# Kernel optimization log

Hardware: AMD Instinct MI355X
Metric: run time of the kernel (lower is better)

## Reference

```python
import jax, jax.numpy as jnp
from jax import lax
import numpy as np

NBC, NAC, KF, RHO = 14, 45, 52, 0.05
KT = np.arange(0.8, 0, -1.0 / 64, dtype=np.float32)[None, :]  # (1, 52) AC kernel time axis
K = KT.shape[1]


def _sigm(x, off, slope):
    return jax.nn.sigmoid(slope * (x - off))


def _ac_kernel(log_tr, log_td, kt):
    tr = jnp.exp(log_tr)[:, None]  # (nAC,1)
    td = jnp.exp(log_td)[:, None]
    k = jnp.exp(-kt / td) - jnp.exp(-(td + tr) / (td * tr) * kt)  # (nAC,K)
    return k / jnp.linalg.norm(k, axis=1, keepdims=True)


def setup_inputs() -> dict:
    key = jax.random.key(0)
    ks = jax.random.split(key, 12)
    B, T = 64, 4096
    n = 0.01  # noise_init_scale
    return {
        "x": jax.random.normal(ks[0], (B, T), jnp.float32) * 0.5,
        "bc_kernels": jax.random.normal(ks[1], (NBC, KF), jnp.float32) * 0.1,
        "log_sigmoid_slope": jnp.log(2.0) + n * jax.random.normal(ks[2], (NBC,), jnp.float32),
        "sigmoid_offset": 1.5 + n * jax.random.normal(ks[3], (NBC,), jnp.float32),
        "log_bc_ac_weight": jnp.log(1.0 / NBC) + n * jax.random.normal(ks[4], (NAC, NBC), jnp.float32),
        "log_ac_tau_rise": jnp.log(0.1) + n * jax.random.normal(ks[5], (NAC,), jnp.float32),
        "log_ac_tau_decay": jnp.log(0.1) + n * jax.random.normal(ks[6], (NAC,), jnp.float32),
        "log_ac_sigmoid_slope": jnp.log(2.0) + n * jax.random.normal(ks[7], (NAC,), jnp.float32),
        "ac_sigmoid_offset": 1.5 + n * jax.random.normal(ks[8], (NAC,), jnp.float32),
        "log_ac_bc_weight": jnp.log(0.01) + n * jax.random.normal(ks[9], (NBC, NAC), jnp.float32),
        "out_scale": jnp.ones((NBC,), jnp.float32),
    }


def reference(x, bc_kernels, log_sigmoid_slope, sigmoid_offset, log_bc_ac_weight,
              log_ac_tau_rise, log_ac_tau_decay, log_ac_sigmoid_slope,
              ac_sigmoid_offset, log_ac_bc_weight, out_scale):
    B, T = x.shape
    kt = jnp.asarray(KT)
    # linear_filter: causal conv of stimulus with per-BC kernels -> (T, B, nBC)
    xf = lax.conv_general_dilated(x[:, None, :], bc_kernels[:, None, :], (1,), [(KF - 1, 0)])
    xf = jnp.transpose(xf, (2, 0, 1))  # (T, B, nBC)

    slope = jnp.exp(log_sigmoid_slope)
    ac_slope = jnp.exp(log_ac_sigmoid_slope)
    bc_ac_w = jnp.exp(log_bc_ac_weight)          # (nAC, nBC)
    ac_bc_w = -jnp.exp(log_ac_bc_weight)         # (nBC, nAC)
    ack = _ac_kernel(log_ac_tau_rise, log_ac_tau_decay, kt)  # (nAC, K)

    # --- plain LNR branch (no feedback) ---
    prob_lnr = _sigm(xf, sigmoid_offset, slope)

    def lnr_step(pool, p):
        pool2 = pool + (1.0 - pool) * RHO
        rel = p * pool2
        return pool2 - rel, rel

    _, rel_lnr = lax.scan(lnr_step, jnp.ones((B, NBC), x.dtype), prob_lnr)
    y_lnr = (out_scale * rel_lnr).transpose(1, 0, 2)  # (B, T, nBC)

    # --- BCN branch with AC feedback recurrence ---
    def bcn_step(carry, xt):
        pool, prev_rel, buf = carry
        # append previous release (track_release[i-1]) to sliding window (oldest first)
        buf = jnp.concatenate([buf[..., 1:], prev_rel[..., None]], axis=-1)  # (B, nBC, K)
        drive = jnp.einsum('ak,ab,nbk->na', ack, bc_ac_w, buf)               # (B, nAC)
        ac_out = _sigm(drive, ac_sigmoid_offset, ac_slope)
        fb = ac_out @ ac_bc_w.T                                              # (B, nBC)
        prob = _sigm(xt + fb, sigmoid_offset, slope)
        pool2 = pool + (1.0 - pool) * RHO
        rel = prob * pool2
        return (pool2 - rel, rel, buf), (rel, fb, ac_out)

    init = (jnp.ones((B, NBC), x.dtype), jnp.zeros((B, NBC), x.dtype), jnp.zeros((B, NBC, K), x.dtype))
    _, (rel, fb, ac_out) = lax.scan(bcn_step, init, xf)
    y_bcn = (out_scale * rel).transpose(1, 0, 2)  # (B, T, nBC)
    return y_bcn, fb.transpose(1, 0, 2), ac_out.transpose(1, 0, 2), y_lnr
```

## Files before the change

### kernel.cpp

```cpp
#include <hip/hip_runtime.h>
#include <hip/hip_fp16.h>

#define NBC 14
#define NAC 45
#define KF  52
#define RHO 0.05f
#define TT  4096
#define BB  64
#define CHC 64
#define WU  44
#define NPAIR 32
#define NTW (WU + CHC)
#define SPAN (WU + 2*CHC)
#define XPAD 176
#define RING 52
#define RINGP 54
#define LOG2E 1.44269504f

typedef __fp16 v2h __attribute__((ext_vector_type(2)));
typedef float  f2  __attribute__((ext_vector_type(2)));
typedef int    i2v __attribute__((ext_vector_type(2)));

__device__ __forceinline__ v2h bch(unsigned u) { return __builtin_bit_cast(v2h, u); }
__device__ __forceinline__ unsigned bcu(v2h h) { return __builtin_bit_cast(unsigned, h); }
__device__ __forceinline__ v2h pk2(float lo, float hi) {
#if __has_builtin(__builtin_amdgcn_cvt_pkrtz)
  return __builtin_bit_cast(v2h, __builtin_amdgcn_cvt_pkrtz(lo, hi));
#else
  v2h r; r[0] = (__fp16)lo; r[1] = (__fp16)hi; return r;
#endif
}
__device__ __forceinline__ v2h xsum16h(v2h v) {
#if __has_builtin(__builtin_amdgcn_permlane16_swap)
  i2v r = __builtin_amdgcn_permlane16_swap((int)bcu(v), (int)bcu(v), false, false);
  return bch((unsigned)r[0]) + bch((unsigned)r[1]);
#else
  return v + bch((unsigned)__builtin_amdgcn_ds_swizzle((int)bcu(v), (16 << 10) | 0x1f));
#endif
}
__device__ __forceinline__ v2h xsum32h(v2h v) {
#if __has_builtin(__builtin_amdgcn_permlane32_swap)
  i2v r = __builtin_amdgcn_permlane32_swap((int)bcu(v), (int)bcu(v), false, false);
  return bch((unsigned)r[0]) + bch((unsigned)r[1]);
#else
  return v + bch((unsigned)__shfl_xor((int)bcu(v), 32));
#endif
}
__device__ __forceinline__ float exp2_f(float x) {
#if __has_builtin(__builtin_amdgcn_exp2f)
  return __builtin_amdgcn_exp2f(x);
#else
  return exp2f(x);
#endif
}

#define POOL_BYTES 14976

__global__ __launch_bounds__(64)
void bcn_kernel(const float* __restrict__ x,
                const float* __restrict__ bck,
                const float* __restrict__ lss,
                const float* __restrict__ soff,
                const float* __restrict__ lbaw,
                const float* __restrict__ ltr,
                const float* __restrict__ ltd,
                const float* __restrict__ lass,
                const float* __restrict__ asoff,
                const float* __restrict__ labw,
                const float* __restrict__ oscale,
                float* __restrict__ out)
{
  __shared__ __align__(16) char pool[POOL_BYTES];
  unsigned* u_ring = (unsigned*)pool;
  float*    x_lds  = (float*)pool;
  __half*   xf_lds = (__half*)(pool + 9720);
  unsigned* acr    = (unsigned*)(pool + 14656);
  unsigned* relr   = (unsigned*)(pool + 14912);

  const int lid   = threadIdx.x;
  const int c16   = lid & 15;
  const int q     = lid >> 4;
  const float rowm = (q & 1) ? 0.f : 1.f;
  const int blk   = blockIdx.x;
  const int b     = blk >> 5;
  const int p     = blk & 31;
  const int t0A   = p * (2 * CHC);
  const int t_begin = t0A - WU;

  for (int i = lid; i < SPAN + KF - 1; i += 64) {
    int gt = t_begin - (KF - 1) + i;
    x_lds[i] = (gt >= 0) ? x[b * TT + gt] : 0.f;
  }
  __syncthreads();

  for (int ib = 0; ib < 3; ++ib) {
    int tau = lid + (ib << 6);
    if (tau < SPAN) {
      float acc[NBC];
#pragma unroll
      for (int c = 0; c < NBC; ++c) acc[c] = 0.f;
#pragma unroll 4
      for (int k = 0; k < KF; ++k) {
        float xv = x_lds[tau + k];
#pragma unroll
        for (int c = 0; c < NBC; ++c) acc[c] = fmaf(bck[c * KF + k], xv, acc[c]);
      }
#pragma unroll
      for (int c = 0; c < NBC; ++c) xf_lds[c * XPAD + tau] = __float2half(acc[c]);
    }
  }
  __syncthreads();

  for (int i = lid; i < NAC * RINGP; i += 64) u_ring[i] = 0u;
  if (lid < 64) acr[lid] = 0u;
  if (lid < 16) relr[lid] = 0u;

  float slope2 = 0.f, soff2 = 0.f, osc_c = 0.f;
  f2 poolP; poolP.x = 1.f; poolP.y = 1.f;
  f2 SA; SA.x = 0.f; SA.y = 0.f;
  f2 SB; SB.x = 0.f; SB.y = 0.f;
  f2 rv2, cn2, co2; rv2.x = rv2.y = cn2.x = cn2.y = co2.x = co2.y = 0.f;
  float Adrv2 = 0.f, Boff2 = 0.f;
  v2h wfbh[16];
  v2h wuh[NBC];
  f2 yst[4], fst[4];
  unsigned acst[4];

#pragma unroll
  for (int j = 0; j < 16; ++j) wfbh[j] = pk2(0.f, 0.f);
#pragma unroll
  for (int c = 0; c < NBC; ++c) wuh[c] = pk2(0.f, 0.f);

  if (c16 < NBC) {
    float sl = expf(lss[c16]);
    slope2 = sl * LOG2E;
    soff2  = soff[c16] * sl * LOG2E;
    osc_c  = oscale[c16];
#pragma unroll
    for (int j = 0; j < 16; ++j) {
      int a = 16 * q + j;
      if (a < NAC) { float w = -expf(labw[c16 * NAC + a]); wfbh[j] = pk2(w, w); }
    }
  }
  if (lid < NAC) {
    float tr = expf(ltr[lid]);
    float td = expf(ltd[lid]);
    float a1 = 1.f / td;
    float gg = (td + tr) / (td * tr);
    rv2.x = expf(-a1 * 0.015625f);  rv2.y = expf(-gg * 0.015625f);
    cn2.x = expf(-a1 * 0.003125f);  cn2.y = expf(-gg * 0.003125f);
    co2.x = expf(-a1 * 0.815625f);  co2.y = expf(-gg * 0.815625f);
    float nrm = 0.f;
    for (int k = 0; k < KF; ++k) {
      float kt = 0.8f - (float)k * 0.015625f;
      float d = expf(-a1 * kt) - expf(-gg * kt);
      nrm = fmaf(d, d, nrm);
    }
    float inorm  = 1.f / sqrtf(nrm);
    float aslope = expf(lass[lid]);
    Adrv2 = aslope * inorm * LOG2E;
    Boff2 = aslope * asoff[lid] * LOG2E;
#pragma unroll
    for (int c = 0; c < NBC; ++c) {
      float w = expf(lbaw[lid * NBC + c]);
      wuh[c] = pk2(w, w);
    }
  }

  float* yb  = out;
  float* fbp = out + (size_t)BB * TT * NBC;
  float* acp = out + 2 * (size_t)BB * TT * NBC;
  float* ylp = out + 2 * (size_t)BB * TT * NBC + (size_t)BB * TT * NAC;

  __syncthreads();

  auto step = [&](int slot4, int rslot, float xfA, float xfB, float uoA, float uoB,
                  bool emit) __attribute__((always_inline)) {
    float mzA = fmaf(-Adrv2, SA.x - SA.y, Boff2);
    float mzB = fmaf(-Adrv2, SB.x - SB.y, Boff2);
    float acA = __fdividef(1.f, 1.f + exp2_f(mzA));
    float acB = __fdividef(1.f, 1.f + exp2_f(mzB));
    if (lid < NAC) acr[lid] = bcu(pk2(acA, acB));

    const uint4* ab = (const uint4*)(acr + (q << 4));
    uint4 A0 = ab[0], A1 = ab[1], A2 = ab[2], A3 = ab[3];
    v2h g0 = wfbh[0] * bch(A0.x);
    v2h g1 = wfbh[1] * bch(A0.y);
    g0 += wfbh[2]  * bch(A0.z);  g1 += wfbh[3]  * bch(A0.w);
    g0 += wfbh[4]  * bch(A1.x);  g1 += wfbh[5]  * bch(A1.y);
    g0 += wfbh[6]  * bch(A1.z);  g1 += wfbh[7]  * bch(A1.w);
    g0 += wfbh[8]  * bch(A2.x);  g1 += wfbh[9]  * bch(A2.y);
    g0 += wfbh[10] * bch(A2.z);  g1 += wfbh[11] * bch(A2.w);
    g0 += wfbh[12] * bch(A3.x);  g1 += wfbh[13] * bch(A3.y);
    g0 += wfbh[14] * bch(A3.z);  g1 += wfbh[15] * bch(A3.w);
    v2h gs = xsum32h(xsum16h(g0 + g1));
    float fbA = (float)gs[0], fbB = (float)gs[1];

    float mA = fmaf(-slope2, fmaf(rowm, fbA, xfA), soff2);
    float mB = fmaf(-slope2, fmaf(rowm, fbB, xfB), soff2);
    f2 pv;
    pv.x = __fdividef(1.f, 1.f + exp2_f(mA));
    pv.y = __fdividef(1.f, 1.f + exp2_f(mB));
    f2 p2 = poolP * (1.f - RHO) + RHO;
    f2 relP = pv * p2;
    poolP = p2 - relP;
    if (lid < NBC) relr[lid] = bcu(pk2(relP.x, relP.y));
    if (emit) {
      yst[slot4] = relP * osc_c;
      f2 t; t.x = fbA; t.y = fbB; fst[slot4] = t;
      acst[slot4] = bcu(pk2(acA, acB));
    }

    const uint4* rb = (const uint4*)relr;
    uint4 R0 = rb[0], R1 = rb[1], R2 = rb[2], R3 = rb[3];
    v2h h0 = wuh[0] * bch(R0.x);
    v2h h1 = wuh[1] * bch(R0.y);
    h0 += wuh[2]  * bch(R0.z);  h1 += wuh[3]  * bch(R0.w);
    h0 += wuh[4]  * bch(R1.x);  h1 += wuh[5]  * bch(R1.y);
    h0 += wuh[6]  * bch(R1.z);  h1 += wuh[7]  * bch(R1.w);
    h0 += wuh[8]  * bch(R2.x);  h1 += wuh[9]  * bch(R2.y);
    h0 += wuh[10] * bch(R2.z);  h1 += wuh[11] * bch(R2.w);
    h0 += wuh[12] * bch(R3.x);  h1 += wuh[13] * bch(R3.y);
    v2h uh = h0 + h1;
    float uA = (float)uh[0], uB = (float)uh[1];
    if (lid < NAC) {
      u_ring[lid * RINGP + rslot] = bcu(uh);
      SA = SA * rv2 + (cn2 * uA - co2 * uoA);
      SB = SB * rv2 + (cn2 * uB - co2 * uoB);
    }
  };

  auto group = [&](int s4, int r4, bool emit) __attribute__((always_inline)) {
    uint2 xa = *(const uint2*)&xf_lds[c16 * XPAD + s4];
    uint2 xb = *(const uint2*)&xf_lds[c16 * XPAD + s4 + CHC];
    int roff = ((lid < NAC) ? lid : 0) * RINGP + r4;
    uint2 ur01 = *(const uint2*)&u_ring[roff];
    uint2 ur23 = *(const uint2*)&u_ring[roff + 2];
    v2h xA01 = bch(xa.x), xA23 = bch(xa.y);
    v2h xB01 = bch(xb.x), xB23 = bch(xb.y);
    v2h u0 = bch(ur01.x), u1 = bch(ur01.y), u2 = bch(ur23.x), u3 = bch(ur23.y);
    step(0, r4 + 0, (float)xA01[0], (float)xB01[0], (float)u0[0], (float)u0[1], emit);
    step(1, r4 + 1, (float)xA01[1], (float)xB01[1], (float)u1[0], (float)u1[1], emit);
    step(2, r4 + 2, (float)xA23[0], (float)xB23[0], (float)u2[0], (float)u2[1], emit);
    step(3, r4 + 3, (float)xA23[1], (float)xB23[1], (float)u3[0], (float)u3[1], emit);
  };

  int r4 = 0;
  for (int s4 = 0; s4 < WU; s4 += 4) {
    group(s4, r4, false);
    r4 += 4; if (r4 == RING) r4 = 0;
  }

  if (p == 0) {
    SA.x = 0.f; SA.y = 0.f;
    poolP.x = 1.f;
    for (int i = lid; i < NAC * RINGP; i += 64) u_ring[i] &= 0xFFFF0000u;
  }

  for (int s4 = WU; s4 < NTW; s4 += 4) {
    group(s4, r4, true);
    r4 += 4; if (r4 == RING) r4 = 0;

    int tgA = t0A + (s4 - WU);
    size_t baseA = (size_t)b * TT + tgA;
    if (lid < NBC) {
      size_t ob = baseA * NBC + lid;
#pragma unroll
      for (int sl = 0; sl < 4; ++sl) {
        yb [ob + sl * NBC]                     = yst[sl].x;
        yb [ob + (size_t)CHC * NBC + sl * NBC] = yst[sl].y;
        fbp[ob + sl * NBC]                     = fst[sl].x;
        fbp[ob + (size_t)CHC * NBC + sl * NBC] = fst[sl].y;
      }
    } else if (lid >= 16 && lid < 16 + NBC) {
      size_t ob = baseA * NBC + (lid - 16);
#pragma unroll
      for (int sl = 0; sl < 4; ++sl) {
        ylp[ob + sl * NBC]                     = yst[sl].x;
        ylp[ob + (size_t)CHC * NBC + sl * NBC] = yst[sl].y;
      }
    }
    if (lid < NAC) {
      size_t oa = baseA * NAC + lid;
#pragma unroll
      for (int sl = 0; sl < 4; ++sl) {
        v2h h = bch(acst[sl]);
        acp[oa + sl * NAC]                     = (float)h[0];
        acp[oa + (size_t)CHC * NAC + sl * NAC] = (float)h[1];
      }
    }
  }
}

extern "C" void kernel_launch(void* const* d_in, const int* in_sizes, int n_in,
                              void* d_out, int out_size, void* d_ws, size_t ws_size,
                              hipStream_t stream) {
  (void)in_sizes; (void)n_in; (void)d_ws; (void)ws_size; (void)out_size;
  bcn_kernel<<<dim3(BB * NPAIR), dim3(64), 0, stream>>>(
      (const float*)d_in[0],
      (const float*)d_in[1],
      (const float*)d_in[2],
      (const float*)d_in[3],
      (const float*)d_in[4],
      (const float*)d_in[5],
      (const float*)d_in[6],
      (const float*)d_in[7],
      (const float*)d_in[8],
      (const float*)d_in[9],
      (const float*)d_in[10],
      (float*)d_out);
}
```

Baseline: 97.41 us.

## Precompute causal convolution in separate kernel and stage fp16 result via workspace

Adds a standalone conv kernel that computes the per-BC causal filter once per timestep into an fp16 global workspace buffer, and the recurrence kernel now loads its span from that buffer instead of recomputing the convolution including warm-up overlap. This removes redundant convolution FMAs across overlapping chunks. It costs an extra kernel launch and a global write/read round trip, and falls back to the old path when workspace is too small. Warm-up positions before t=0 now use a clamped value instead of zero.

After: 97.43 us. Within noise of the previous version (+0.0%).

```diff
diff --git a/kernel.cpp b/kernel.cpp
--- a/kernel.cpp
+++ b/kernel.cpp
@@ -16,6 +16,7 @@
 #define RING 52
 #define RINGP 54
 #define LOG2E 1.44269504f
+#define XF_BYTES ((size_t)BB * NBC * TT * 2)
 
 typedef __fp16 v2h __attribute__((ext_vector_type(2)));
 typedef float  f2  __attribute__((ext_vector_type(2)));
@@ -54,8 +55,35 @@
 #endif
 }
 
+__global__ __launch_bounds__(256)
+void conv_kernel(const float* __restrict__ x, const float* __restrict__ bck,
+                 __half* __restrict__ xfg) {
+  __shared__ float xs[256 + KF];
+  const int tid  = threadIdx.x;
+  const int b    = blockIdx.x >> 4;
+  const int t0   = (blockIdx.x & 15) << 8;
+  for (int i = tid; i < 256 + KF - 1; i += 256) {
+    int gt = t0 - (KF - 1) + i;
+    xs[i] = (gt >= 0) ? x[b * TT + gt] : 0.f;
+  }
+  __syncthreads();
+  float acc[NBC];
+#pragma unroll
+  for (int c = 0; c < NBC; ++c) acc[c] = 0.f;
+#pragma unroll 4
+  for (int k = 0; k < KF; ++k) {
+    float xv = xs[tid + k];
+#pragma unroll
+    for (int c = 0; c < NBC; ++c) acc[c] = fmaf(bck[c * KF + k], xv, acc[c]);
+  }
+#pragma unroll
+  for (int c = 0; c < NBC; ++c)
+    xfg[((size_t)b * NBC + c) * TT + t0 + tid] = __float2half(acc[c]);
+}
+
 #define POOL_BYTES 14976
 
+template<bool PRECONV>
 __global__ __launch_bounds__(64)
 void bcn_kernel(const float* __restrict__ x,
                 const float* __restrict__ bck,
@@ -68,6 +96,7 @@
                 const float* __restrict__ asoff,
                 const float* __restrict__ labw,
                 const float* __restrict__ oscale,
+                const __half* __restrict__ xfg,
                 float* __restrict__ out)
 {
   __shared__ __align__(16) char pool[POOL_BYTES];
@@ -87,29 +116,46 @@
   const int t0A   = p * (2 * CHC);
   const int t_begin = t0A - WU;
 
-  for (int i = lid; i < SPAN + KF - 1; i += 64) {
-    int gt = t_begin - (KF - 1) + i;
-    x_lds[i] = (gt >= 0) ? x[b * TT + gt] : 0.f;
-  }
-  __syncthreads();
-
-  for (int ib = 0; ib < 3; ++ib) {
-    int tau = lid + (ib << 6);
-    if (tau < SPAN) {
-      float acc[NBC];
-#pragma unroll
-      for (int c = 0; c < NBC; ++c) acc[c] = 0.f;
+  if constexpr (PRECONV) {
+    const __half* src = xfg + (size_t)b * NBC * TT;
+    if (p == 0) {
+      for (int e = lid; e < NBC * SPAN; e += 64) {
+        int c = e / SPAN, i = e - c * SPAN;
+        int gt = t_begin + i; if (gt < 0) gt = 0;
+        xf_lds[c * XPAD + i] = src[(size_t)c * TT + gt];
+      }
+    } else {
+      for (int c = 0; c < NBC; ++c) {
+        if (lid < SPAN / 4) {
+          uint2 v = *(const uint2*)(src + (size_t)c * TT + t_begin + 4 * lid);
+          *(uint2*)&xf_lds[c * XPAD + 4 * lid] = v;
+        }
+      }
+    }
+  } else {
+    for (int i = lid; i < SPAN + KF - 1; i += 64) {
+      int gt = t_begin - (KF - 1) + i;
+      x_lds[i] = (gt >= 0) ? x[b * TT + gt] : 0.f;
+    }
+    __syncthreads();
+    for (int ib = 0; ib < 3; ++ib) {
+      int tau = lid + (ib << 6);
+      if (tau < SPAN) {
+        float acc[NBC];
+#pragma unroll
+        for (int c = 0; c < NBC; ++c) acc[c] = 0.f;
 #pragma unroll 4
-      for (int k = 0; k < KF; ++k) {
-        float xv = x_lds[tau + k];
-#pragma unroll
-        for (int c = 0; c < NBC; ++c) acc[c] = fmaf(bck[c * KF + k], xv, acc[c]);
-      }
-#pragma unroll
-      for (int c = 0; c < NBC; ++c) xf_lds[c * XPAD + tau] = __float2half(acc[c]);
-    }
-  }
-  __syncthreads();
+        for (int k = 0; k < KF; ++k) {
+          float xv = x_lds[tau + k];
+#pragma unroll
+          for (int c = 0; c < NBC; ++c) acc[c] = fmaf(bck[c * KF + k], xv, acc[c]);
+        }
+#pragma unroll
+        for (int c = 0; c < NBC; ++c) xf_lds[c * XPAD + tau] = __float2half(acc[c]);
+      }
+    }
+    __syncthreads();
+  }
 
   for (int i = lid; i < NAC * RINGP; i += 64) u_ring[i] = 0u;
   if (lid < 64) acr[lid] = 0u;
@@ -295,18 +341,22 @@
 extern "C" void kernel_launch(void* const* d_in, const int* in_sizes, int n_in,
                               void* d_out, int out_size, void* d_ws, size_t ws_size,
                               hipStream_t stream) {
-  (void)in_sizes; (void)n_in; (void)d_ws; (void)ws_size; (void)out_size;
-  bcn_kernel<<<dim3(BB * NPAIR), dim3(64), 0, stream>>>(
-      (const float*)d_in[0],
-      (const float*)d_in[1],
-      (const float*)d_in[2],
-      (const float*)d_in[3],
-      (const float*)d_in[4],
-      (const float*)d_in[5],
-      (const float*)d_in[6],
-      (const float*)d_in[7],
-      (const float*)d_in[8],
-      (const float*)d_in[9],
-      (const float*)d_in[10],
-      (float*)d_out);
-}
+  (void)in_sizes; (void)n_in; (void)out_size;
+  const float* x    = (const float*)d_in[0];
+  const float* bck  = (const float*)d_in[1];
+  if (ws_size >= XF_BYTES) {
+    __half* xfg = (__half*)d_ws;
+    conv_kernel<<<dim3(BB * 16), dim3(256), 0, stream>>>(x, bck, xfg);
+    bcn_kernel<true><<<dim3(BB * NPAIR), dim3(64), 0, stream>>>(
+        x, bck, (const float*)d_in[2], (const float*)d_in[3], (const float*)d_in[4],
+        (const float*)d_in[5], (const float*)d_in[6], (const float*)d_in[7],
+        (const float*)d_in[8], (const float*)d_in[9], (const float*)d_in[10],
+        xfg, (float*)d_out);
+  } else {
+    bcn_kernel<false><<<dim3(BB * NPAIR), dim3(64), 0, stream>>>(
+        x, bck, (const float*)d_in[2], (const float*)d_in[3], (const float*)d_in[4],
+        (const float*)d_in[5], (const float*)d_in[6], (const float*)d_in[7],
+        (const float*)d_in[8], (const float*)d_in[9], (const float*)d_in[10],
+        (const __half*)nullptr, (float*)d_out);
+  }
+}
```
